# Optimization experiments

Measured on AMD Instinct MI355X. Metric: run time of the kernel, lower is better.

## Reference

```python
import jax, jax.numpy as jnp
import numpy as np

B, S, T, C = 8, 25, 75, 5  # tasks, support per task, targets per task, classes per set
CAP = S // C               # fixed slot capacity used by the torch scatter buffer
EPS = 1e-8


def _conv(x, W, b):
    # x: [N, Cin, H, W], W: [Cout, Cin, 3, 3] (OIHW), stride 2, SAME padding
    y = jax.lax.conv_general_dilated(
        x, W, window_strides=(2, 2), padding='SAME',
        dimension_numbers=('NCHW', 'OIHW', 'NCHW'))
    return jax.nn.relu(y + b[None, :, None, None])


def _encode(x, W1, b1, W2, b2, W3, b3, W4, b4):
    # Conv4 backbone: 84 -> 42 -> 21 -> 11 -> 6 spatial, 64 channels
    x = _conv(x, W1, b1)
    x = _conv(x, W2, b2)
    x = _conv(x, W3, b3)
    x = _conv(x, W4, b4)
    return x.reshape(x.shape[0], -1)  # [N, 2304]


def setup_inputs() -> dict:
    key = jax.random.key(0)
    ks = jax.random.split(key, 8)
    inp = {
        'x_support_set': jax.random.normal(ks[0], (B, S, 3, 84, 84), jnp.float32),
        'x_target_set': jax.random.normal(ks[1], (B, T, 3, 84, 84), jnp.float32),
        # arange labels -> y % C is perfectly class-balanced per task (CAP each)
        'y_support_set': jnp.arange(B * S, dtype=jnp.int32).reshape(B, S),
        'W1': jax.random.normal(ks[2], (64, 3, 3, 3), jnp.float32) * 0.1,
        'b1': jnp.zeros((64,), jnp.float32),
        'W2': jax.random.normal(ks[3], (64, 64, 3, 3), jnp.float32) * 0.05,
        'b2': jnp.zeros((64,), jnp.float32),
        'W3': jax.random.normal(ks[4], (64, 64, 3, 3), jnp.float32) * 0.05,
        'b3': jnp.zeros((64,), jnp.float32),
        'W4': jax.random.normal(ks[5], (64, 64, 3, 3), jnp.float32) * 0.05,
        'b4': jnp.zeros((64,), jnp.float32),
    }
    return inp


def reference(x_support_set, x_target_set, y_support_set,
              W1, b1, W2, b2, W3, b3, W4, b4):
    # Encode support set: [B*S, 3, 84, 84] -> [B, S, D]
    emb_s = _encode(x_support_set.reshape(-1, 3, 84, 84),
                    W1, b1, W2, b2, W3, b3, W4, b4).reshape(B, S, -1)
    # Per-class prototypes: torch builds a zero buffer [C, CAP, D], scatters each
    # embedding into slot (y % C), then .mean(1). With balanced labels that is a
    # segment-sum over classes divided by the fixed capacity CAP.
    onehot = jax.nn.one_hot(y_support_set % C, C, dtype=emb_s.dtype)  # [B, S, C]
    protos = jnp.einsum('bsc,bsd->bcd', onehot, emb_s) / CAP          # [B, C, D]
    # Encode target set: [B, T, D]
    emb_t = _encode(x_target_set.reshape(-1, 3, 84, 84),
                    W1, b1, W2, b2, W3, b3, W4, b4).reshape(B, T, -1)
    # Cosine-similarity logits (matching-network classification head)
    tn = emb_t / jnp.maximum(jnp.linalg.norm(emb_t, axis=-1, keepdims=True), EPS)
    pn = protos / jnp.maximum(jnp.linalg.norm(protos, axis=-1, keepdims=True), EPS)
    preds = jnp.einsum('btd,bcd->btc', tn, pn)  # [B, T, C]
    return preds
```

## Files before the change

### kernel.cpp

```cpp
#include <hip/hip_runtime.h>
#include <hip/hip_bf16.h>


#define BB 8
#define SS 25
#define TT 75
#define CC 5
#define DD 2304
#define NSUP 200
#define NTGT 600
#define NTOT 800
#define EPSF 1e-8f

#define PLE 7744
#define IMG1E 123904

typedef __attribute__((ext_vector_type(8))) short bf16x8;
typedef __attribute__((ext_vector_type(4))) float f32x4;

__device__ __forceinline__ float load_ext(const void* p, size_t idx, int isf32) {
  if (isf32) return ((const float*)p)[idx];
  unsigned short u = ((const unsigned short*)p)[idx];
  union { unsigned int i; float f; } v;
  v.i = ((unsigned int)u) << 16;
  return v.f;
}

__global__ void fsc_probe_dtype_k(const unsigned short* __restrict__ w2raw,
                                  int nelems, int* __restrict__ flag) {
  __shared__ int cnt;
  if (threadIdx.x == 0) cnt = 0;
  __syncthreads();
  int local = 0;
  for (int i = threadIdx.x; i < nelems; i += 256) {
    unsigned short u = w2raw[i];
    int ex = (u >> 7) & 0xFF;
    if (ex != 0 && (ex < 0x69 || ex > 0x84)) local++;
  }
  atomicAdd(&cnt, local);
  __syncthreads();
  if (threadIdx.x == 0) *flag = (cnt > nelems / 8) ? 1 : 0;
}

__global__ void fsc_repack_w1m_k(const void* __restrict__ W,
                                 __hip_bfloat16* __restrict__ Wf,
                                 const int* __restrict__ flag) {
  const int isf32 = *flag;
  int i = blockIdx.x * blockDim.x + threadIdx.x;
  if (i >= 4096) return;
  int j = i & 7;
  int lane = (i >> 3) & 63;
  int t = (i >> 9) & 3;
  int s = i >> 11;
  int kk = (lane >> 4) * 8 + j;
  int co = t * 16 + (lane & 15);
  float v = 0.f;
  int kh, kwp, ci;
  bool live = false;
  if (s == 0) { kh = kk >> 4; kwp = (kk & 15) >> 2; ci = kk & 3; live = true; }
  else if (kk < 16) { kh = 2; kwp = kk >> 2; ci = kk & 3; live = true; }
  if (live && kwp < 3 && ci < 3)
    v = load_ext(W, (size_t)((co * 3 + ci) * 3 + kh) * 3 + kwp, isf32);
  Wf[i] = __float2bfloat16(v);
}

__global__ void fsc_repack_wm_k(const void* __restrict__ W,
                                __hip_bfloat16* __restrict__ Wf,
                                const int* __restrict__ flag) {
  const int isf32 = *flag;
  int o = blockIdx.x * blockDim.x + threadIdx.x;
  if (o >= 36864) return;
  int j = o & 7;
  int lane = (o >> 3) & 63;
  int t = (o >> 9) & 3;
  int kk = o >> 11;
  int s = kk & 1;
  int khw = kk >> 1;
  int kh = khw / 3, kw = khw - kh * 3;
  int co = t * 16 + (lane & 15);
  int ci = s * 32 + (lane >> 4) * 8 + j;
  float v = load_ext(W, (size_t)((co * 64 + ci) * 3 + kh) * 3 + kw, isf32);
  Wf[o] = __float2bfloat16(v);
}

template <int P>
__global__ void fsc_zero_border_k(__hip_bfloat16* __restrict__ buf, int N) {
  int i = blockIdx.x * blockDim.x + threadIdx.x;
  const int RP = 4 * P - 4;
  if (i >= N * RP * 64) return;
  int c = i & 63;
  int r = (i >> 6) % RP;
  int n = (i >> 6) / RP;
  int row, colp;
  if (r < P) { row = 0; colp = r; }
  else if (r < 2 * P) { row = P - 1; colp = r - P; }
  else if (r < 3 * P - 2) { row = r - 2 * P + 1; colp = 0; }
  else { row = r - (3 * P - 2) + 1; colp = P - 1; }
  buf[(((size_t)n * P + row) * P + colp) * 64 + c] = __float2bfloat16(0.f);
}

__global__ void fsc_zero_a1p_k(__hip_bfloat16* __restrict__ A1, int N) {
  int i = blockIdx.x * blockDim.x + threadIdx.x;
  if (i >= N * 16 * 86 * 8) return;
  int ch = i & 7;
  int q = (i >> 3) % 86;
  int pl = ((i >> 3) / 86) % 16;
  int n = (i >> 3) / (86 * 16);
  const int wp = pl & 1;
  int h, w2;
  if (q < 22) { h = 0; w2 = q; }
  else if (q < 44) { h = 43; w2 = q - 22; }
  else { h = q - 43; w2 = wp ? 21 : 0; }
  A1[(size_t)n * IMG1E + pl * PLE + (h * 22 + w2) * 8 + ch] = __float2bfloat16(0.f);
}

__global__ void fsc_zero_xb_k(__hip_bfloat16* __restrict__ X, int N) {
  int i = blockIdx.x * blockDim.x + threadIdx.x;
  if (i >= N * 1360) return;
  int c = i & 3;
  int p = (i >> 2) % 340;
  int n = (i >> 2) / 340;
  int h, w;
  if (p < 172) { h = 84 + (p / 86); w = p % 86; }
  else { int pp = p - 172; h = pp >> 1; w = 84 + (pp & 1); }
  X[(((size_t)n * 86 + h) * 86 + w) * 4 + c] = __float2bfloat16(0.f);
}

__global__ void fsc_xform1_k(const void* __restrict__ x, int srcImg0,
                             __hip_bfloat16* __restrict__ X, int dstImg0,
                             int n, const int* __restrict__ flag) {
  const int isf32 = *flag;
  int i = blockIdx.x * blockDim.x + threadIdx.x;
  const int imgL = i / 7056;
  if (imgL >= n) return;
  const int sp = i - imgL * 7056;
  const int h = sp / 84, w = sp - h * 84;
  const size_t base = (size_t)(srcImg0 + imgL) * 21168;
  union { unsigned short u[4]; uint2 q; } pk;
#pragma unroll
  for (int ci = 0; ci < 3; ++ci)
    pk.u[ci] = __bfloat16_as_ushort(__float2bfloat16(load_ext(x, base + ci * 7056 + sp, isf32)));
  pk.u[3] = 0;
  *(uint2*)(void*)(X + (((size_t)(dstImg0 + imgL) * 86 + h) * 86 + w) * 4) = pk.q;
}

__global__ void fsc_conv1m_k(const __hip_bfloat16* __restrict__ X,
                             const __hip_bfloat16* __restrict__ Wf,
                             const void* __restrict__ bias,
                             __hip_bfloat16* __restrict__ out, int N,
                             const int* __restrict__ flag) {
  constexpr int TPI = 28;
  const int wid = blockIdx.x * 4 + (threadIdx.x >> 6);
  const int img = wid / TPI;
  if (img >= N) return;
  const int tl = wid - img * TPI;
  const int lane = threadIdx.x & 63;
  const int nidx = lane & 15, quad = lane >> 4;

  int col[4];
  bool val[4];
  int hoA[4], woA[4];
#pragma unroll
  for (int p = 0; p < 4; ++p) {
    col[p] = tl * 64 + p * 16 + nidx;
    val[p] = col[p] < 1764;
    if (!val[p]) col[p] = 1763;
    hoA[p] = col[p] / 42;
    woA[p] = col[p] - hoA[p] * 42;
  }

  f32x4 acc[4][4];
#pragma unroll
  for (int p = 0; p < 4; ++p)
#pragma unroll
    for (int t = 0; t < 4; ++t) acc[p][t] = (f32x4){0.f, 0.f, 0.f, 0.f};

#pragma unroll
  for (int s = 0; s < 2; ++s) {
    bf16x8 b[4];
#pragma unroll
    for (int p = 0; p < 4; ++p) {
      const int hi = 2 * hoA[p] + (s == 0 ? (quad >> 1) : 2);
      const __hip_bfloat16* bp =
          X + (((size_t)img * 86 + hi) * 86 + 2 * woA[p]) * 4 + (quad & 1) * 8;
      b[p] = *(const bf16x8*)(const void*)bp;
    }
#pragma unroll
    for (int t = 0; t < 4; ++t) {
      bf16x8 a = *(const bf16x8*)(const void*)(Wf + ((size_t)(s * 4 + t) * 64 + lane) * 8);
#pragma unroll
      for (int p = 0; p < 4; ++p)
        acc[p][t] = __builtin_amdgcn_mfma_f32_16x16x32_bf16(a, b[p], acc[p][t], 0, 0, 0);
    }
  }

  const int isf32 = *flag;
#pragma unroll
  for (int p = 0; p < 4; ++p) {
    const int h = hoA[p] + 1;
    const int wq = woA[p] + 1;
    const int wp = wq & 1, w2 = wq >> 1;
#pragma unroll
    for (int t = 0; t < 4; ++t) {
      float v[4];
#pragma unroll
      for (int r = 0; r < 4; ++r) {
        const int cout = t * 16 + quad * 4 + r;
        float xv = acc[p][t][r] + load_ext(bias, cout, isf32);
        v[r] = xv > 0.f ? xv : 0.f;
      }
      if (val[p]) {
        __hip_bfloat16* o = out + (size_t)img * IMG1E +
                            ((2 * t + (quad >> 1)) * 2 + wp) * PLE +
                            (h * 22 + w2) * 8 + (quad & 1) * 4;
        union { unsigned short u[4]; uint2 w; } pk;
#pragma unroll
        for (int r = 0; r < 4; ++r) pk.u[r] = __bfloat16_as_ushort(__float2bfloat16(v[r]));
        *(uint2*)(void*)o = pk.w;
      }
    }
  }
}

__global__ void fsc_conv2p_k(const __hip_bfloat16* __restrict__ A1,
                             const __hip_bfloat16* __restrict__ Wf,
                             const void* __restrict__ bias,
                             __hip_bfloat16* __restrict__ out, int N,
                             const int* __restrict__ flag) {
  constexpr int TPI = 14;
  const int wid = blockIdx.x * 4 + (threadIdx.x >> 6);
  const int img = wid / TPI;
  if (img >= N) return;
  const int tl = wid - img * TPI;
  const int lane = threadIdx.x & 63;
  const int nidx = lane & 15, quad = lane >> 4;

  int col[2];
  bool val[2];
  int hoA[2], woA[2];
  const __hip_bfloat16* bsrc[2];
#pragma unroll
  for (int p = 0; p < 2; ++p) {
    col[p] = tl * 32 + p * 16 + nidx;
    val[p] = col[p] < 441;
    if (!val[p]) col[p] = 440;
    hoA[p] = col[p] / 21;
    woA[p] = col[p] - hoA[p] * 21;
    bsrc[p] = A1 + (size_t)img * IMG1E + quad * (2 * PLE) +
              ((2 * hoA[p] + 1) * 22 + woA[p]) * 8;
  }
  const __hip_bfloat16* asrc = Wf + lane * 8;

  f32x4 acc[2][4];
#pragma unroll
  for (int p = 0; p < 2; ++p)
#pragma unroll
    for (int t = 0; t < 4; ++t) acc[p][t] = (f32x4){0.f, 0.f, 0.f, 0.f};

#define FSC_BOFF2(kk)                                                        \
  ((((kk)&1) * 8 + ((1 + (((kk) >> 1) % 3)) & 1)) * PLE +                    \
   (((((kk) >> 1)) / 3) * 22 + ((1 + (((kk) >> 1) % 3)) >> 1)) * 8)

  bf16x8 bbuf[4][2];
#pragma unroll
  for (int d = 0; d < 3; ++d)
#pragma unroll
    for (int p = 0; p < 2; ++p)
      bbuf[d][p] = *(const bf16x8*)(const void*)(bsrc[p] + FSC_BOFF2(d));

#pragma unroll
  for (int kk = 0; kk < 18; ++kk) {
    if (kk + 3 < 18) {
#pragma unroll
      for (int p = 0; p < 2; ++p)
        bbuf[(kk + 3) & 3][p] =
            *(const bf16x8*)(const void*)(bsrc[p] + FSC_BOFF2(kk + 3));
    }
#pragma unroll
    for (int t = 0; t < 4; ++t) {
      bf16x8 a = *(const bf16x8*)(const void*)(asrc + (kk * 4 + t) * 512);
#pragma unroll
      for (int p = 0; p < 2; ++p)
        acc[p][t] =
            __builtin_amdgcn_mfma_f32_16x16x32_bf16(a, bbuf[kk & 3][p], acc[p][t], 0, 0, 0);
    }
  }
#undef FSC_BOFF2

  const int isf32 = *flag;
#pragma unroll
  for (int p = 0; p < 2; ++p) {
#pragma unroll
    for (int t = 0; t < 4; ++t) {
      float v[4];
#pragma unroll
      for (int r = 0; r < 4; ++r) {
        const int cout = t * 16 + quad * 4 + r;
        float xv = acc[p][t][r] + load_ext(bias, cout, isf32);
        v[r] = xv > 0.f ? xv : 0.f;
      }
      if (val[p]) {
        __hip_bfloat16* o = out + (((size_t)img * 23 + (hoA[p] + 1)) * 23 +
                                   (woA[p] + 1)) * 64 + t * 16 + quad * 4;
        union { unsigned short u[4]; uint2 w; } pk;
#pragma unroll
        for (int r = 0; r < 4; ++r) pk.u[r] = __bfloat16_as_ushort(__float2bfloat16(v[r]));
        *(uint2*)(void*)o = pk.w;
      }
    }
  }
}

template <int HO, int PWI, int PWO, int ROFF, int CG>
__global__ void fsc_convp_k(const __hip_bfloat16* __restrict__ in,
                            const __hip_bfloat16* __restrict__ Wf,
                            const void* __restrict__ bias,
                            __hip_bfloat16* __restrict__ out, int N,
                            const int* __restrict__ flag) {
  constexpr int COLS = CG * 16;
  constexpr int TPI = (HO * HO + COLS - 1) / COLS;
  const int wid = blockIdx.x * 4 + (threadIdx.x >> 6);
  const int img = wid / TPI;
  if (img >= N) return;
  const int tl = wid - img * TPI;
  const int lane = threadIdx.x & 63;
  const int nidx = lane & 15, quad = lane >> 4;

  int col[CG];
  bool val[CG];
  int hoA[CG], woA[CG];
  const __hip_bfloat16* bsrc[CG];
#pragma unroll
  for (int p = 0; p < CG; ++p) {
    col[p] = tl * COLS + p * 16 + nidx;
    val[p] = col[p] < HO * HO;
    if (!val[p]) col[p] = HO * HO - 1;
    hoA[p] = col[p] / HO;
    woA[p] = col[p] - hoA[p] * HO;
    bsrc[p] = in + (((size_t)img * PWI + (2 * hoA[p] + ROFF)) * PWI +
                    (2 * woA[p] + ROFF)) * 64 + quad * 8;
  }
  const __hip_bfloat16* asrc = Wf + lane * 8;

  f32x4 acc[CG][4];
#pragma unroll
  for (int p = 0; p < CG; ++p)
#pragma unroll
    for (int t = 0; t < 4; ++t) acc[p][t] = (f32x4){0.f, 0.f, 0.f, 0.f};

#define FSC_BOFF(kk) ((((kk) >> 1) / 3 * PWI + ((kk) >> 1) % 3) * 64 + ((kk)&1) * 32)

  bf16x8 bbuf[4][CG];
#pragma unroll
  for (int d = 0; d < 3; ++d)
#pragma unroll
    for (int p = 0; p < CG; ++p)
      bbuf[d][p] = *(const bf16x8*)(const void*)(bsrc[p] + FSC_BOFF(d));

#pragma unroll
  for (int kk = 0; kk < 18; ++kk) {
    if (kk + 3 < 18) {
#pragma unroll
      for (int p = 0; p < CG; ++p)
        bbuf[(kk + 3) & 3][p] =
            *(const bf16x8*)(const void*)(bsrc[p] + FSC_BOFF(kk + 3));
    }
#pragma unroll
    for (int t = 0; t < 4; ++t) {
      bf16x8 a = *(const bf16x8*)(const void*)(asrc + (kk * 4 + t) * 512);
#pragma unroll
      for (int p = 0; p < CG; ++p)
        acc[p][t] =
            __builtin_amdgcn_mfma_f32_16x16x32_bf16(a, bbuf[kk & 3][p], acc[p][t], 0, 0, 0);
    }
  }
#undef FSC_BOFF

  const int isf32 = *flag;
#pragma unroll
  for (int p = 0; p < CG; ++p) {
#pragma unroll
    for (int t = 0; t < 4; ++t) {
      float v[4];
#pragma unroll
      for (int r = 0; r < 4; ++r) {
        const int cout = t * 16 + quad * 4 + r;
        float xv = acc[p][t][r] + load_ext(bias, cout, isf32);
        v[r] = xv > 0.f ? xv : 0.f;
      }
      if (val[p]) {
        __hip_bfloat16* o = out + (((size_t)img * PWO + (hoA[p] + 1)) * PWO +
                                   (woA[p] + 1)) * 64 + t * 16 + quad * 4;
        union { unsigned short u[4]; uint2 w; } pk;
#pragma unroll
        for (int r = 0; r < 4; ++r) pk.u[r] = __bfloat16_as_ushort(__float2bfloat16(v[r]));
        *(uint2*)(void*)o = pk.w;
      }
    }
  }
}

__global__ void fsc_conv4_k(const __hip_bfloat16* __restrict__ in,
                            const __hip_bfloat16* __restrict__ Wf,
                            const void* __restrict__ bias, float* __restrict__ emb,
                            int N, const int* __restrict__ flag) {
  constexpr int HO = 6, PWI = 13;
  constexpr int TPI = 2;
  const int wid = blockIdx.x * 4 + (threadIdx.x >> 6);
  const int img = wid / TPI;
  if (img >= N) return;
  const int tl = wid - img * TPI;
  const int lane = threadIdx.x & 63;
  const int nidx = lane & 15, quad = lane >> 4;

  int col0 = tl * 32 + nidx;
  int col1 = col0 + 16;
  const bool val0 = col0 < HO * HO;
  const bool val1 = col1 < HO * HO;
  if (!val0) col0 = HO * HO - 1;
  if (!val1) col1 = HO * HO - 1;
  const int ho0 = col0 / HO, wo0 = col0 - ho0 * HO;
  const int ho1 = col1 / HO, wo1 = col1 - ho1 * HO;

  const __hip_bfloat16* bsrc0 =
      in + (((size_t)img * PWI + 2 * ho0) * PWI + 2 * wo0) * 64 + quad * 8;
  const __hip_bfloat16* bsrc1 =
      in + (((size_t)img * PWI + 2 * ho1) * PWI + 2 * wo1) * 64 + quad * 8;
  const __hip_bfloat16* asrc = Wf + lane * 8;

  f32x4 acc[2][4];
#pragma unroll
  for (int p = 0; p < 2; ++p)
#pragma unroll
    for (int t = 0; t < 4; ++t) acc[p][t] = (f32x4){0.f, 0.f, 0.f, 0.f};

#pragma unroll
  for (int kk = 0; kk < 18; ++kk) {
    const int s = kk & 1;
    const int khw = kk >> 1;
    const int kh = khw / 3, kw = khw - kh * 3;
    const int boff = (kh * PWI + kw) * 64 + s * 32;
    bf16x8 b0 = *(const bf16x8*)(const void*)(bsrc0 + boff);
    bf16x8 b1 = *(const bf16x8*)(const void*)(bsrc1 + boff);
#pragma unroll
    for (int t = 0; t < 4; ++t) {
      bf16x8 a = *(const bf16x8*)(const void*)(asrc + (kk * 4 + t) * 512);
      acc[0][t] = __builtin_amdgcn_mfma_f32_16x16x32_bf16(a, b0, acc[0][t], 0, 0, 0);
      acc[1][t] = __builtin_amdgcn_mfma_f32_16x16x32_bf16(a, b1, acc[1][t], 0, 0, 0);
    }
  }

  const int isf32 = *flag;
#pragma unroll
  for (int p = 0; p < 2; ++p) {
    const bool valid = p == 0 ? val0 : val1;
    const int col = p == 0 ? col0 : col1;
#pragma unroll
    for (int t = 0; t < 4; ++t) {
      float v[4];
#pragma unroll
      for (int r = 0; r < 4; ++r) {
        const int cout = t * 16 + quad * 4 + r;
        float xv = acc[p][t][r] + load_ext(bias, cout, isf32);
        v[r] = xv > 0.f ? xv : 0.f;
      }
      if (valid) {
        float* o = emb + ((size_t)img * 36 + col) * 64 + t * 16 + quad * 4;
        *(f32x4*)(void*)o = (f32x4){v[0], v[1], v[2], v[3]};
      }
    }
  }
}

__global__ void fsc_proto_k(const float* __restrict__ emb_s, const int* __restrict__ y,
                            float* __restrict__ protos) {
  int i = blockIdx.x * blockDim.x + threadIdx.x;
  if (i >= BB * CC * DD) return;
  int d = i % DD;
  int bc = i / DD;
  int c = bc % CC;
  int b = bc / CC;
  float sum = 0.f;
  for (int s = 0; s < SS; ++s) {
    if (y[b * SS + s] % CC == c) sum += emb_s[(size_t)(b * SS + s) * DD + d];
  }
  protos[i] = sum * 0.2f;
}

__global__ void fsc_pnorm_k(const float* __restrict__ protos, float* __restrict__ pn) {
  __shared__ float red[4];
  __shared__ float inv;
  const int bc = blockIdx.x;
  const float* p = protos + (size_t)bc * DD;
  float ss = 0.f;
  for (int d = threadIdx.x; d < DD; d += 256) { float v = p[d]; ss += v * v; }
#pragma unroll
  for (int off = 32; off > 0; off >>= 1) ss += __shfl_down(ss, off);
  if ((threadIdx.x & 63) == 0) red[threadIdx.x >> 6] = ss;
  __syncthreads();
  if (threadIdx.x == 0) {
    float nrm = sqrtf(red[0] + red[1] + red[2] + red[3]);
    nrm = nrm > EPSF ? nrm : EPSF;
    inv = 1.f / nrm;
  }
  __syncthreads();
  float sc = inv;
  for (int d = threadIdx.x; d < DD; d += 256) pn[(size_t)bc * DD + d] = p[d] * sc;
}

__global__ void fsc_preds_k(const float* __restrict__ emb_t, const float* __restrict__ pn,
                            void* __restrict__ out, const int* __restrict__ flag) {
  __shared__ float red[4][6];
  __shared__ float fin[6];
  const int isf32 = *flag;
  const int bt = blockIdx.x;
  const int b = bt / TT;
  const float* et = emb_t + (size_t)bt * DD;
  float e[9];
#pragma unroll
  for (int k = 0; k < 9; ++k) e[k] = et[threadIdx.x + 256 * k];
  float vals[6];
  {
    float ss = 0.f;
#pragma unroll
    for (int k = 0; k < 9; ++k) ss += e[k] * e[k];
    vals[0] = ss;
  }
  const float* pb = pn + (size_t)b * CC * DD;
#pragma unroll
  for (int c = 0; c < CC; ++c) {
    float s = 0.f;
#pragma unroll
    for (int k = 0; k < 9; ++k) s += e[k] * pb[(size_t)c * DD + threadIdx.x + 256 * k];
    vals[1 + c] = s;
  }
#pragma unroll
  for (int v = 0; v < 6; ++v) {
#pragma unroll
    for (int off = 32; off > 0; off >>= 1) vals[v] += __shfl_down(vals[v], off);
  }
  if ((threadIdx.x & 63) == 0) {
#pragma unroll
    for (int v = 0; v < 6; ++v) red[threadIdx.x >> 6][v] = vals[v];
  }
  __syncthreads();
  if (threadIdx.x < 6)
    fin[threadIdx.x] = red[0][threadIdx.x] + red[1][threadIdx.x] +
                       red[2][threadIdx.x] + red[3][threadIdx.x];
  __syncthreads();
  if (threadIdx.x < CC) {
    float nt = sqrtf(fin[0]);
    nt = nt > EPSF ? nt : EPSF;
    float r = fin[1 + threadIdx.x] / nt;
    if (isf32) ((float*)out)[(size_t)bt * CC + threadIdx.x] = r;
    else ((__hip_bfloat16*)out)[(size_t)bt * CC + threadIdx.x] = __float2bfloat16(r);
  }
}

static inline int fsc_cdiv(int a, int b) { return (a + b - 1) / b; }
static inline int imin(int a, int b) { return a < b ? a : b; }
static inline int imax(int a, int b) { return a > b ? a : b; }

extern "C" void kernel_launch(void* const* d_in, const int* in_sizes, int n_in,
                              void* d_out, int out_size, void* d_ws, size_t ws_size,
                              hipStream_t stream) {
  const void* xs = d_in[0];
  const void* xt = d_in[1];
  const int* y = (const int*)d_in[2];
  const void* W1 = d_in[3];
  const void* b1 = d_in[4];
  const void* W2 = d_in[5];
  const void* b2 = d_in[6];
  const void* W3 = d_in[7];
  const void* b3 = d_in[8];
  const void* W4 = d_in[9];
  const void* b4 = d_in[10];

  char* w = (char*)d_ws;
  int* flag = (int*)w;                      w += 256;
  __hip_bfloat16* Wf1 = (__hip_bfloat16*)w; w += 4096 * 2;
  __hip_bfloat16* Wf2 = (__hip_bfloat16*)w; w += 36864 * 2;
  __hip_bfloat16* Wf3 = (__hip_bfloat16*)w; w += 36864 * 2;
  __hip_bfloat16* Wf4 = (__hip_bfloat16*)w; w += 36864 * 2;
  float* protos = (float*)w;                w += (size_t)BB * CC * DD * 4;
  float* pn = (float*)w;                    w += (size_t)BB * CC * DD * 4;
  float* emb = (float*)w;                   w += (size_t)NTOT * DD * 4;
  __hip_bfloat16* C3 = (__hip_bfloat16*)w;  w += (size_t)NTOT * 13 * 13 * 64 * 2;
  char* chunk0 = w;
  const size_t fixedB = (size_t)(w - (char*)d_ws);
  const size_t szX  = (size_t)86 * 86 * 4 * 2;
  const size_t szA1 = (size_t)IMG1E * 2;
  const size_t szA2 = (size_t)23 * 23 * 64 * 2;
  const size_t perImgB = szX + szA1 + szA2;

  int CH = 50;
  const int cands[7] = {640, 600, 512, 400, 200, 100, 50};
  for (int k = 0; k < 7; ++k) {
    if (fixedB + (size_t)cands[k] * perImgB <= ws_size) { CH = cands[k]; break; }
  }
  __hip_bfloat16* X  = (__hip_bfloat16*)chunk0;
  __hip_bfloat16* A1 = (__hip_bfloat16*)(chunk0 + (size_t)CH * szX);
  __hip_bfloat16* A2 = (__hip_bfloat16*)(chunk0 + (size_t)CH * (szX + szA1));

  fsc_probe_dtype_k<<<1, 256, 0, stream>>>((const unsigned short*)W2, 64 * 64 * 9, flag);
  fsc_repack_w1m_k<<<fsc_cdiv(4096, 256), 256, 0, stream>>>(W1, Wf1, flag);
  fsc_repack_wm_k<<<fsc_cdiv(36864, 256), 256, 0, stream>>>(W2, Wf2, flag);
  fsc_repack_wm_k<<<fsc_cdiv(36864, 256), 256, 0, stream>>>(W3, Wf3, flag);
  fsc_repack_wm_k<<<fsc_cdiv(36864, 256), 256, 0, stream>>>(W4, Wf4, flag);

  fsc_zero_xb_k<<<fsc_cdiv(CH * 1360, 256), 256, 0, stream>>>(X, CH);
  fsc_zero_a1p_k<<<fsc_cdiv(CH * 16 * 86 * 8, 256), 256, 0, stream>>>(A1, CH);
  fsc_zero_border_k<23><<<fsc_cdiv(CH * (4 * 23 - 4) * 64, 256), 256, 0, stream>>>(A2, CH);
  fsc_zero_border_k<13><<<fsc_cdiv(NTOT * (4 * 13 - 4) * 64, 256), 256, 0, stream>>>(C3, NTOT);

  for (int g0 = 0; g0 < NTOT; g0 += CH) {
    const int n = imin(CH, NTOT - g0);
    if (g0 < NSUP) {
      const int cnt = imin(g0 + n, NSUP) - g0;
      fsc_xform1_k<<<fsc_cdiv(cnt * 7056, 256), 256, 0, stream>>>(
          xs, g0, X, 0, cnt, flag);
    }
    if (g0 + n > NSUP) {
      const int tStart = imax(g0, NSUP);
      const int cnt = g0 + n - tStart;
      fsc_xform1_k<<<fsc_cdiv(cnt * 7056, 256), 256, 0, stream>>>(
          xt, tStart - NSUP, X, tStart - g0, cnt, flag);
    }
    fsc_conv1m_k<<<fsc_cdiv(n * 28, 4), 256, 0, stream>>>(X, Wf1, b1, A1, n, flag);
    fsc_conv2p_k<<<fsc_cdiv(n * 14, 4), 256, 0, stream>>>(A1, Wf2, b2, A2, n, flag);
    fsc_convp_k<11, 23, 13, 0, 1><<<fsc_cdiv(n * 8, 4), 256, 0, stream>>>(
        A2, Wf3, b3, C3 + (size_t)g0 * 13 * 13 * 64, n, flag);
  }

  fsc_conv4_k<<<fsc_cdiv(NTOT * 2, 4), 256, 0, stream>>>(C3, Wf4, b4, emb, NTOT, flag);

  fsc_proto_k<<<fsc_cdiv(BB * CC * DD, 256), 256, 0, stream>>>(emb, y, protos);
  fsc_pnorm_k<<<BB * CC, 256, 0, stream>>>(protos, pn);
  fsc_preds_k<<<NTGT, 256, 0, stream>>>(emb + (size_t)NSUP * DD, pn, d_out, flag);
}
```

Before: 429.6 us.

## Stage conv2 input rows in LDS and drop register prefetch in conv3

```diff
diff --git a/kernel.cpp b/kernel.cpp
--- a/kernel.cpp
+++ b/kernel.cpp
@@ -222,32 +222,43 @@
   }
 }
 
-__global__ void fsc_conv2p_k(const __hip_bfloat16* __restrict__ A1,
+__global__ void fsc_conv2l_k(const __hip_bfloat16* __restrict__ A1,
                              const __hip_bfloat16* __restrict__ Wf,
                              const void* __restrict__ bias,
                              __hip_bfloat16* __restrict__ out, int N,
                              const int* __restrict__ flag) {
-  constexpr int TPI = 14;
-  const int wid = blockIdx.x * 4 + (threadIdx.x >> 6);
-  const int img = wid / TPI;
+  __shared__ __hip_bfloat16 sb[30976];
+  const int bid = blockIdx.x;
+  const int img = bid / 5;
   if (img >= N) return;
-  const int tl = wid - img * TPI;
-  const int lane = threadIdx.x & 63;
+  const int r0 = (bid - img * 5) * 4;
+  const int tid = threadIdx.x;
+
+  for (int c = tid; c < 3872; c += 256) {
+    const int pl = c / 242;
+    const int rem = c - pl * 242;
+    const int hL = rem / 22;
+    const int w2 = rem - hL * 22;
+    const __hip_bfloat16* src = A1 + (size_t)img * IMG1E + pl * PLE +
+                                ((2 * r0 + 1 + hL) * 22 + w2) * 8;
+    *(uint4*)(void*)(sb + (size_t)c * 8) = *(const uint4*)(const void*)src;
+  }
+  __syncthreads();
+
+  const int wv = tid >> 6;
+  const int lane = tid & 63;
   const int nidx = lane & 15, quad = lane >> 4;
 
   int col[2];
   bool val[2];
-  int hoA[2], woA[2];
-  const __hip_bfloat16* bsrc[2];
+  int hoL[2], woA[2];
 #pragma unroll
   for (int p = 0; p < 2; ++p) {
-    col[p] = tl * 32 + p * 16 + nidx;
-    val[p] = col[p] < 441;
-    if (!val[p]) col[p] = 440;
-    hoA[p] = col[p] / 21;
-    woA[p] = col[p] - hoA[p] * 21;
-    bsrc[p] = A1 + (size_t)img * IMG1E + quad * (2 * PLE) +
-              ((2 * hoA[p] + 1) * 22 + woA[p]) * 8;
+    col[p] = wv * 32 + p * 16 + nidx;
+    val[p] = col[p] < 105;
+    if (!val[p]) col[p] = 104;
+    hoL[p] = col[p] / 21;
+    woA[p] = col[p] - hoL[p] * 21;
   }
   const __hip_bfloat16* asrc = Wf + lane * 8;
 
@@ -257,39 +268,32 @@
 #pragma unroll
     for (int t = 0; t < 4; ++t) acc[p][t] = (f32x4){0.f, 0.f, 0.f, 0.f};
 
-#define FSC_BOFF2(kk)                                                        \
-  ((((kk)&1) * 8 + ((1 + (((kk) >> 1) % 3)) & 1)) * PLE +                    \
-   (((((kk) >> 1)) / 3) * 22 + ((1 + (((kk) >> 1) % 3)) >> 1)) * 8)
-
-  bf16x8 bbuf[4][2];
-#pragma unroll
-  for (int d = 0; d < 3; ++d)
-#pragma unroll
-    for (int p = 0; p < 2; ++p)
-      bbuf[d][p] = *(const bf16x8*)(const void*)(bsrc[p] + FSC_BOFF2(d));
-
 #pragma unroll
   for (int kk = 0; kk < 18; ++kk) {
-    if (kk + 3 < 18) {
+    const int s = kk & 1;
+    const int khw = kk >> 1;
+    const int kh = khw / 3, kw = khw - kh * 3;
+    const int wp = (1 + kw) & 1, dw2 = (1 + kw) >> 1;
+    bf16x8 b[2];
+#pragma unroll
+    for (int p = 0; p < 2; ++p) {
+      const int off = (((8 * s + 2 * quad + wp) * 11 + (2 * hoL[p] + kh)) * 22 +
+                       woA[p] + dw2) * 8;
+      b[p] = *(const bf16x8*)(const void*)(sb + off);
+    }
+#pragma unroll
+    for (int t = 0; t < 4; ++t) {
+      bf16x8 a = *(const bf16x8*)(const void*)(asrc + (kk * 4 + t) * 512);
 #pragma unroll
       for (int p = 0; p < 2; ++p)
-        bbuf[(kk + 3) & 3][p] =
-            *(const bf16x8*)(const void*)(bsrc[p] + FSC_BOFF2(kk + 3));
-    }
-#pragma unroll
-    for (int t = 0; t < 4; ++t) {
-      bf16x8 a = *(const bf16x8*)(const void*)(asrc + (kk * 4 + t) * 512);
-#pragma unroll
-      for (int p = 0; p < 2; ++p)
-        acc[p][t] =
-            __builtin_amdgcn_mfma_f32_16x16x32_bf16(a, bbuf[kk & 3][p], acc[p][t], 0, 0, 0);
-    }
-  }
-#undef FSC_BOFF2
+        acc[p][t] = __builtin_amdgcn_mfma_f32_16x16x32_bf16(a, b[p], acc[p][t], 0, 0, 0);
+    }
+  }
 
   const int isf32 = *flag;
 #pragma unroll
   for (int p = 0; p < 2; ++p) {
+    const int ho = r0 + hoL[p];
 #pragma unroll
     for (int t = 0; t < 4; ++t) {
       float v[4];
@@ -300,7 +304,7 @@
         v[r] = xv > 0.f ? xv : 0.f;
       }
       if (val[p]) {
-        __hip_bfloat16* o = out + (((size_t)img * 23 + (hoA[p] + 1)) * 23 +
+        __hip_bfloat16* o = out + (((size_t)img * 23 + (ho + 1)) * 23 +
                                    (woA[p] + 1)) * 64 + t * 16 + quad * 4;
         union { unsigned short u[4]; uint2 w; } pk;
 #pragma unroll
@@ -348,33 +352,23 @@
 #pragma unroll
     for (int t = 0; t < 4; ++t) acc[p][t] = (f32x4){0.f, 0.f, 0.f, 0.f};
 
-#define FSC_BOFF(kk) ((((kk) >> 1) / 3 * PWI + ((kk) >> 1) % 3) * 64 + ((kk)&1) * 32)
-
-  bf16x8 bbuf[4][CG];
-#pragma unroll
-  for (int d = 0; d < 3; ++d)
-#pragma unroll
-    for (int p = 0; p < CG; ++p)
-      bbuf[d][p] = *(const bf16x8*)(const void*)(bsrc[p] + FSC_BOFF(d));
-
 #pragma unroll
   for (int kk = 0; kk < 18; ++kk) {
-    if (kk + 3 < 18) {
+    const int s = kk & 1;
+    const int khw = kk >> 1;
+    const int kh = khw / 3, kw = khw - kh * 3;
+    const int boff = (kh * PWI + kw) * 64 + s * 32;
+    bf16x8 b[CG];
+#pragma unroll
+    for (int p = 0; p < CG; ++p) b[p] = *(const bf16x8*)(const void*)(bsrc[p] + boff);
+#pragma unroll
+    for (int t = 0; t < 4; ++t) {
+      bf16x8 a = *(const bf16x8*)(const void*)(asrc + (kk * 4 + t) * 512);
 #pragma unroll
       for (int p = 0; p < CG; ++p)
-        bbuf[(kk + 3) & 3][p] =
-            *(const bf16x8*)(const void*)(bsrc[p] + FSC_BOFF(kk + 3));
-    }
-#pragma unroll
-    for (int t = 0; t < 4; ++t) {
-      bf16x8 a = *(const bf16x8*)(const void*)(asrc + (kk * 4 + t) * 512);
-#pragma unroll
-      for (int p = 0; p < CG; ++p)
-        acc[p][t] =
-            __builtin_amdgcn_mfma_f32_16x16x32_bf16(a, bbuf[kk & 3][p], acc[p][t], 0, 0, 0);
-    }
-  }
-#undef FSC_BOFF
+        acc[p][t] = __builtin_amdgcn_mfma_f32_16x16x32_bf16(a, b[p], acc[p][t], 0, 0, 0);
+    }
+  }
 
   const int isf32 = *flag;
 #pragma unroll
@@ -627,7 +621,7 @@
           xt, tStart - NSUP, X, tStart - g0, cnt, flag);
     }
     fsc_conv1m_k<<<fsc_cdiv(n * 28, 4), 256, 0, stream>>>(X, Wf1, b1, A1, n, flag);
-    fsc_conv2p_k<<<fsc_cdiv(n * 14, 4), 256, 0, stream>>>(A1, Wf2, b2, A2, n, flag);
+    fsc_conv2l_k<<<n * 5, 256, 0, stream>>>(A1, Wf2, b2, A2, n, flag);
     fsc_convp_k<11, 23, 13, 0, 1><<<fsc_cdiv(n * 8, 4), 256, 0, stream>>>(
         A2, Wf3, b3, C3 + (size_t)g0 * 13 * 13 * 64, n, flag);
   }
```

Result: slower. 497.3 us (+15.8%).
